# Performance work log

Measured on AMD Instinct MI355X. Metric: run time of the kernel, lower is better.

The kernel has to match this reference:

```python
import jax, jax.numpy as jnp
import numpy as np

B, N, D, H = 8, 1024, 768, 12
HD = D // H  # head_dim = 64


def setup_inputs() -> dict:
    key = jax.random.key(0)
    k1, k2 = jax.random.split(key)
    x = jax.random.normal(k1, (B, N, D), dtype=jnp.float32)
    W_qkv = jax.random.normal(k2, (D, 3 * D), dtype=jnp.float32) * 0.02
    b_qkv = jnp.zeros((3 * D,), dtype=jnp.float32)
    return {"x": x, "W_qkv": W_qkv, "b_qkv": b_qkv}


def reference(x, W_qkv, b_qkv):
    b, n, d = x.shape
    qkv = x @ W_qkv + b_qkv                      # [B, N, 3D]
    qkv = qkv.reshape(b, n, 3, H, HD)
    qkv = jnp.transpose(qkv, (2, 0, 3, 1, 4))    # [3, B, H, N, HD]
    q, k, v = qkv[0], qkv[1], qkv[2]
    scale = 1.0 / jnp.sqrt(jnp.float32(HD))
    scores = jnp.einsum('bhqd,bhkd->bhqk', q, k) * scale   # [B, H, N, N]
    attn = jax.nn.softmax(scores, axis=-1)
    out = jnp.einsum('bhqk,bhkd->bhqd', attn, v)            # [B, H, N, HD]
    # concat heads along last dim (same as torch.cat over head outputs)
    return jnp.transpose(out, (0, 2, 1, 3)).reshape(b, n, d)
```

## Files before the change

kernel.cpp:

```cpp
#include <hip/hip_runtime.h>
#include <stdint.h>

#define BB 8
#define NN 1024
#define DDIM 768
#define HH 12
#define HDIM 64
#define D3 2304
#define MM 8192

typedef __attribute__((ext_vector_type(4))) float f32x4;
typedef __attribute__((ext_vector_type(16))) float f32x16;
typedef __attribute__((ext_vector_type(8))) __bf16 bf16x8;
typedef __attribute__((ext_vector_type(8))) unsigned short u16x8;
typedef __attribute__((ext_vector_type(4))) unsigned short u16x4;

__device__ __forceinline__ unsigned short f2bf(float f) {
  unsigned int u = __float_as_uint(f);
  u += 0x7FFFu + ((u >> 16) & 1u);
  return (unsigned short)(u >> 16);
}

__device__ __forceinline__ void gload_lds16(const void* g, void* l) {
  __builtin_amdgcn_global_load_lds((const __attribute__((address_space(1))) void*)g,
                                   (__attribute__((address_space(3))) void*)l,
                                   16, 0, 0);
}

__device__ __forceinline__ unsigned cvtpk_bf16(float lo, float hi) {
  unsigned r;
  asm("v_cvt_pk_bf16_f32 %0, %1, %2" : "=v"(r) : "v"(lo), "v"(hi));
  return r;
}

__device__ __forceinline__ bf16x8 mkfrag(unsigned a, unsigned b, unsigned c, unsigned d) {
  union { unsigned u[4]; bf16x8 v; } x;
  x.u[0] = a; x.u[1] = b; x.u[2] = c; x.u[3] = d;
  return x.v;
}

#if __has_builtin(__builtin_amdgcn_exp2f)
#define EXP2(x) __builtin_amdgcn_exp2f(x)
#else
#define EXP2(x) exp2f(x)
#endif

#define QSCL 0.18033688f

__global__ void k_prep(const float4* __restrict__ x, u16x4* __restrict__ xb,
                       const float* __restrict__ W, unsigned short* __restrict__ Wt) {
  __shared__ float tile[32][33];
  const int bid = blockIdx.x;
  if (bid < 6144) {
    int i = bid * 256 + threadIdx.x;
    float4 v = x[i];
    u16x4 o;
    o[0] = f2bf(v.x); o[1] = f2bf(v.y); o[2] = f2bf(v.z); o[3] = f2bf(v.w);
    xb[i] = o;
    return;
  }
  const int bid2 = bid - 6144;
  const int tx = threadIdx.x & 31, ty = threadIdx.x >> 5;
  const int n0 = (bid2 % 72) * 32;
  const int k0 = (bid2 / 72) * 32;
  for (int i = 0; i < 4; ++i) {
    int k = k0 + ty + i * 8;
    tile[ty + i * 8][tx] = W[(size_t)k * D3 + n0 + tx];
  }
  __syncthreads();
  for (int i = 0; i < 4; ++i) {
    int n = n0 + ty + i * 8;
    Wt[(size_t)n * DDIM + k0 + tx] = f2bf(tile[tx][ty + i * 8]);
  }
}

__global__ __launch_bounds__(256, 2)
void k_gemm(const unsigned short* __restrict__ A, const unsigned short* __restrict__ Bt,
            const float* __restrict__ bias, unsigned short* __restrict__ qb,
            unsigned short* __restrict__ kp, unsigned short* __restrict__ vp) {
  __shared__ char lds[64 * 1024];
  const int t = threadIdx.x, lane = t & 63, wid = t >> 6;
  const int orig = blockIdx.x;
  const int xcd = orig & 7, tt = orig >> 3;
  const int m0 = (xcd * 8 + (tt & 7)) * 128;
  const int n0 = (tt >> 3) * 128;
  const int wr = wid >> 1, wc = wid & 1;
  const int grp = lane >> 4, lc = lane & 15;

  f32x4 acc[4][4];
  for (int i = 0; i < 4; ++i)
    for (int j = 0; j < 4; ++j) acc[i][j] = (f32x4)(0.0f);

  auto STAGE = [&](int buf, int kt) {
    char* Ab = lds + buf * 32768;
    char* Bb = Ab + 16384;
#pragma unroll
    for (int i = 0; i < 4; ++i) {
      int id = wid * 4 + i;
      int row = id * 8 + (lane >> 3);
      int cs = ((lane & 7) << 4) ^ ((row & 7) << 4);
      gload_lds16((const char*)A + (size_t)(m0 + row) * 1536 + kt * 128 + cs, Ab + id * 1024);
      gload_lds16((const char*)Bt + (size_t)(n0 + row) * 1536 + kt * 128 + cs, Bb + id * 1024);
    }
  };

  STAGE(0, 0);
  for (int kt = 0; kt < 12; ++kt) {
    if (kt < 11) {
      STAGE((kt + 1) & 1, kt + 1);
      asm volatile("s_waitcnt vmcnt(8)" ::: "memory");
    } else {
      asm volatile("s_waitcnt vmcnt(0)" ::: "memory");
    }
    __builtin_amdgcn_s_barrier();

    const char* As = lds + (kt & 1) * 32768;
    const char* Bs = As + 16384;
    bf16x8 af[4][2], bfr[4][2];
#pragma unroll
    for (int f = 0; f < 4; ++f)
#pragma unroll
      for (int kk = 0; kk < 2; ++kk) {
        int ra = wr * 64 + f * 16 + lc;
        af[f][kk] = *(const bf16x8*)(As + ra * 128 + ((kk * 64 + grp * 16) ^ ((ra & 7) << 4)));
        int rb = wc * 64 + f * 16 + lc;
        bfr[f][kk] = *(const bf16x8*)(Bs + rb * 128 + ((kk * 64 + grp * 16) ^ ((rb & 7) << 4)));
      }
    __builtin_amdgcn_s_setprio(1);
#pragma unroll
    for (int mf = 0; mf < 4; ++mf)
#pragma unroll
      for (int nf = 0; nf < 4; ++nf) {
        acc[mf][nf] = __builtin_amdgcn_mfma_f32_16x16x32_bf16(af[mf][0], bfr[nf][0], acc[mf][nf], 0, 0, 0);
        acc[mf][nf] = __builtin_amdgcn_mfma_f32_16x16x32_bf16(af[mf][1], bfr[nf][1], acc[mf][nf], 0, 0, 0);
      }
    __builtin_amdgcn_s_setprio(0);
    __builtin_amdgcn_s_barrier();
  }

  float bv[4];
#pragma unroll
  for (int nf = 0; nf < 4; ++nf) bv[nf] = bias[n0 + wc * 64 + nf * 16 + lc];

  const int nt = n0 >> 7;
  if (nt < 6) {
#pragma unroll
    for (int mf = 0; mf < 4; ++mf)
#pragma unroll
      for (int nf = 0; nf < 4; ++nf)
#pragma unroll
        for (int i = 0; i < 4; ++i) {
          int r = m0 + wr * 64 + mf * 16 + grp * 4 + i;
          int c = n0 + wc * 64 + nf * 16 + lc;
          qb[(size_t)r * DDIM + c] = f2bf((acc[mf][nf][i] + bv[nf]) * QSCL);
        }
  } else {
    __syncthreads();
    unsigned short* lt = (unsigned short*)lds + wid * 4608;
    const int l31 = lane & 31, hi2 = lane >> 5;
    const int bb = m0 >> 10;
    const int kt_ = ((m0 & 1023) >> 6) + wr;
    size_t base;
    unsigned short* dst;
    if (nt < 12) {
      const int h = ((n0 - DDIM) >> 6) + wc;
      base = ((size_t)(bb * HH + h) * 16 + kt_) * 4096;
      dst = kp;
#pragma unroll
      for (int mf = 0; mf < 4; ++mf)
#pragma unroll
        for (int nf = 0; nf < 4; ++nf)
#pragma unroll
          for (int i = 0; i < 4; ++i)
            lt[(mf * 16 + grp * 4 + i) * 72 + nf * 16 + lc] = f2bf(acc[mf][nf][i] + bv[nf]);
    } else {
      const int h = ((n0 - 2 * DDIM) >> 6) + wc;
      base = ((size_t)(bb * HH + h) * 16 + kt_) * 4096;
      dst = vp;
#pragma unroll
      for (int mf = 0; mf < 4; ++mf)
#pragma unroll
        for (int nf = 0; nf < 4; ++nf)
#pragma unroll
          for (int i = 0; i < 4; ++i)
            lt[(nf * 16 + lc) * 72 + mf * 16 + grp * 4 + i] = f2bf(acc[mf][nf][i] + bv[nf]);
    }
    __syncthreads();
#pragma unroll
    for (int c2 = 0; c2 < 4; ++c2)
#pragma unroll
      for (int r = 0; r < 2; ++r)
        *(u16x8*)(dst + base + ((size_t)(c2 * 2 + r) * 64 + lane) * 8) =
          *(const u16x8*)&lt[(r * 32 + l31) * 72 + c2 * 16 + hi2 * 8];
  }
}

__global__ __launch_bounds__(256, 3)
void k_attn(const unsigned short* __restrict__ qb,
            const unsigned short* __restrict__ kp, const unsigned short* __restrict__ vp,
            float* __restrict__ out) {
  __shared__ char lds[32 * 1024];
  const int lane = threadIdx.x & 63, wid = threadIdx.x >> 6;
  const int orig = blockIdx.x;
  const int wg = (orig & 7) * 96 + (orig >> 3);
  const int bh = wg >> 3, qt = wg & 7;
  const int b = bh / HH, h = bh % HH;
  const int q0 = qt * 128 + wid * 32;
  const int l31 = lane & 31, hi = lane >> 5;

  auto STAGE = [&](int bi, int kt2) {
    char* buf = lds + bi * 16384;
    const char* gk = (const char*)kp + (size_t)(bh * 16 + kt2) * 8192 + lane * 16;
    const char* gv = (const char*)vp + (size_t)(bh * 16 + kt2) * 8192 + lane * 16;
#pragma unroll
    for (int i = 0; i < 4; ++i) {
      int e = wid * 4 + i;
      const char* g = (e < 8) ? (gk + e * 1024) : (gv + (e - 8) * 1024);
      char* l = (e < 8) ? (buf + e * 1024) : (buf + 8192 + (e - 8) * 1024);
      gload_lds16(g, l);
    }
  };

  bf16x8 qf[4];
  const char* qbase = (const char*)qb + ((size_t)(b * NN + q0 + l31) * DDIM + h * HDIM) * 2;
#pragma unroll
  for (int ds_ = 0; ds_ < 4; ++ds_)
    qf[ds_] = *(const bf16x8*)(qbase + ds_ * 32 + hi * 16);

  STAGE(0, 0);

  f32x16 acc0 = (f32x16)(0.0f), acc1 = (f32x16)(0.0f);
  float l = 0.0f;

  for (int kt = 0; kt < 16; ++kt) {
    const int cur = kt & 1;
    if (kt < 15) {
      STAGE(cur ^ 1, kt + 1);
      asm volatile("s_waitcnt vmcnt(4)" ::: "memory");
    } else {
      asm volatile("s_waitcnt vmcnt(0)" ::: "memory");
    }
    __builtin_amdgcn_s_barrier();

    const char* Kc = lds + cur * 16384;
    const char* Vc = Kc + 8192;

    bf16x8 kf[4][2];
#pragma unroll
    for (int ds_ = 0; ds_ < 4; ++ds_)
#pragma unroll
      for (int r = 0; r < 2; ++r)
        kf[ds_][r] = *(const bf16x8*)(Kc + (ds_ * 2 + r) * 1024 + lane * 16);

    f32x16 st0 = (f32x16)(0.0f), st1 = (f32x16)(0.0f);
    __builtin_amdgcn_s_setprio(1);
#pragma unroll
    for (int ds_ = 0; ds_ < 4; ++ds_) {
      st0 = __builtin_amdgcn_mfma_f32_32x32x16_bf16(kf[ds_][0], qf[ds_], st0, 0, 0, 0);
      st1 = __builtin_amdgcn_mfma_f32_32x32x16_bf16(kf[ds_][1], qf[ds_], st1, 0, 0, 0);
    }
    __builtin_amdgcn_s_setprio(0);

    bf16x8 vf[4][2];
#pragma unroll
    for (int cc = 0; cc < 4; ++cc)
#pragma unroll
      for (int r = 0; r < 2; ++r)
        vf[cc][r] = *(const bf16x8*)(Vc + (cc * 2 + r) * 1024 + lane * 16);

    float s0 = 0.f, s1 = 0.f, s2 = 0.f, s3 = 0.f;
#pragma unroll
    for (int i = 0; i < 16; i += 4) {
      float p0 = EXP2(st0[i]);
      float p1 = EXP2(st0[i + 1]);
      float p2 = EXP2(st0[i + 2]);
      float p3 = EXP2(st0[i + 3]);
      st0[i] = p0; st0[i + 1] = p1; st0[i + 2] = p2; st0[i + 3] = p3;
      s0 += p0; s1 += p1; s2 += p2; s3 += p3;
    }
#pragma unroll
    for (int i = 0; i < 16; i += 4) {
      float p0 = EXP2(st1[i]);
      float p1 = EXP2(st1[i + 1]);
      float p2 = EXP2(st1[i + 2]);
      float p3 = EXP2(st1[i + 3]);
      st1[i] = p0; st1[i + 1] = p1; st1[i + 2] = p2; st1[i + 3] = p3;
      s0 += p0; s1 += p1; s2 += p2; s3 += p3;
    }
    l += (s0 + s1) + (s2 + s3);

#pragma unroll
    for (int kblk = 0; kblk < 2; ++kblk) {
      const f32x16& sp = kblk ? st1 : st0;
      unsigned c0 = cvtpk_bf16(sp[0], sp[1]),   c1 = cvtpk_bf16(sp[2], sp[3]);
      unsigned c2 = cvtpk_bf16(sp[4], sp[5]),   c3 = cvtpk_bf16(sp[6], sp[7]);
      unsigned c4 = cvtpk_bf16(sp[8], sp[9]),   c5 = cvtpk_bf16(sp[10], sp[11]);
      unsigned c6 = cvtpk_bf16(sp[12], sp[13]), c7 = cvtpk_bf16(sp[14], sp[15]);
      unsigned z0 = hi ? c0 : c2, z1 = hi ? c1 : c3;
      unsigned z2 = hi ? c4 : c6, z3 = hi ? c5 : c7;
      unsigned w0 = __shfl_xor(z0, 32, 64), w1 = __shfl_xor(z1, 32, 64);
      unsigned w2 = __shfl_xor(z2, 32, 64), w3 = __shfl_xor(z3, 32, 64);
      bf16x8 pf0 = mkfrag(hi ? w0 : c0, hi ? w1 : c1, hi ? c2 : w0, hi ? c3 : w1);
      bf16x8 pf1 = mkfrag(hi ? w2 : c4, hi ? w3 : c5, hi ? c6 : w2, hi ? c7 : w3);

      __builtin_amdgcn_s_setprio(1);
#pragma unroll
      for (int ch = 0; ch < 2; ++ch) {
        const int cc = kblk * 2 + ch;
        const bf16x8 pf = ch ? pf1 : pf0;
        acc0 = __builtin_amdgcn_mfma_f32_32x32x16_bf16(vf[cc][0], pf, acc0, 0, 0, 0);
        acc1 = __builtin_amdgcn_mfma_f32_32x32x16_bf16(vf[cc][1], pf, acc1, 0, 0, 0);
      }
      __builtin_amdgcn_s_setprio(0);
    }

    __builtin_amdgcn_s_barrier();
  }

  float lf = l + __shfl_xor(l, 32, 64);
  float inv = 1.0f / lf;
  float* obase = out + (size_t)(b * NN + q0 + l31) * DDIM + h * HDIM + hi * 4;
#pragma unroll
  for (int rq = 0; rq < 4; ++rq) {
    f32x4 o;
    o[0] = acc0[rq * 4] * inv; o[1] = acc0[rq * 4 + 1] * inv;
    o[2] = acc0[rq * 4 + 2] * inv; o[3] = acc0[rq * 4 + 3] * inv;
    *(f32x4*)(obase + rq * 8) = o;
  }
#pragma unroll
  for (int rq = 0; rq < 4; ++rq) {
    f32x4 o;
    o[0] = acc1[rq * 4] * inv; o[1] = acc1[rq * 4 + 1] * inv;
    o[2] = acc1[rq * 4 + 2] * inv; o[3] = acc1[rq * 4 + 3] * inv;
    *(f32x4*)(obase + 32 + rq * 8) = o;
  }
}

extern "C" void kernel_launch(void* const* d_in, const int* in_sizes, int n_in,
                              void* d_out, int out_size, void* d_ws, size_t ws_size,
                              hipStream_t stream) {
  const float* x = (const float*)d_in[0];
  const float* W = (const float*)d_in[1];
  const float* bqkv = (const float*)d_in[2];
  float* out = (float*)d_out;
  char* ws = (char*)d_ws;

  const size_t XB_OFF = 0;
  const size_t WT_OFF = 12582912;
  const size_t QB_OFF = WT_OFF + 3538944;
  const size_t KP_OFF = QB_OFF + 12582912;
  const size_t VP_OFF = KP_OFF + 12582912;
  unsigned short* xb = (unsigned short*)(ws + XB_OFF);
  unsigned short* wt = (unsigned short*)(ws + WT_OFF);
  unsigned short* qbf = (unsigned short*)(ws + QB_OFF);
  unsigned short* kpk = (unsigned short*)(ws + KP_OFF);
  unsigned short* vpk = (unsigned short*)(ws + VP_OFF);

  k_prep<<<dim3(6144 + 1728), dim3(256), 0, stream>>>((const float4*)x, (u16x4*)xb, W, wt);
  k_gemm<<<dim3(1152), dim3(256), 0, stream>>>(xb, wt, bqkv, qbf, kpk, vpk);
  k_attn<<<dim3(768), dim3(256), 0, stream>>>(qbf, kpk, vpk, out);
}
```

Measured before the change: 82.79 us.

## Load K/V fragments directly from global memory instead of LDS double buffering

Removes the LDS double-buffered staging of K and V tiles, along with its barriers and waitcnt handling. Each wave now reads its K and V MFMA fragments straight from global memory, relying on L2/cache reuse across the four waves of a block. The launch bounds hint is also dropped. This removes LDS traffic and block-wide synchronisation, but each wave now issues redundant global loads, and the latency is no longer hidden by explicit prefetch.

Measured after the change: 105.0 us. 26.9% more time.

```diff
diff --git a/kernel.cpp b/kernel.cpp
--- a/kernel.cpp
+++ b/kernel.cpp
@@ -195,11 +195,9 @@
   }
 }
 
-__global__ __launch_bounds__(256, 3)
-void k_attn(const unsigned short* __restrict__ qb,
-            const unsigned short* __restrict__ kp, const unsigned short* __restrict__ vp,
-            float* __restrict__ out) {
-  __shared__ char lds[32 * 1024];
+__global__ void k_attn(const unsigned short* __restrict__ qb,
+                       const unsigned short* __restrict__ kp, const unsigned short* __restrict__ vp,
+                       float* __restrict__ out) {
   const int lane = threadIdx.x & 63, wid = threadIdx.x >> 6;
   const int orig = blockIdx.x;
   const int wg = (orig & 7) * 96 + (orig >> 3);
@@ -208,49 +206,35 @@
   const int q0 = qt * 128 + wid * 32;
   const int l31 = lane & 31, hi = lane >> 5;
 
-  auto STAGE = [&](int bi, int kt2) {
-    char* buf = lds + bi * 16384;
-    const char* gk = (const char*)kp + (size_t)(bh * 16 + kt2) * 8192 + lane * 16;
-    const char* gv = (const char*)vp + (size_t)(bh * 16 + kt2) * 8192 + lane * 16;
-#pragma unroll
-    for (int i = 0; i < 4; ++i) {
-      int e = wid * 4 + i;
-      const char* g = (e < 8) ? (gk + e * 1024) : (gv + (e - 8) * 1024);
-      char* l = (e < 8) ? (buf + e * 1024) : (buf + 8192 + (e - 8) * 1024);
-      gload_lds16(g, l);
-    }
-  };
-
   bf16x8 qf[4];
   const char* qbase = (const char*)qb + ((size_t)(b * NN + q0 + l31) * DDIM + h * HDIM) * 2;
 #pragma unroll
   for (int ds_ = 0; ds_ < 4; ++ds_)
     qf[ds_] = *(const bf16x8*)(qbase + ds_ * 32 + hi * 16);
 
-  STAGE(0, 0);
+  const char* kbase = (const char*)kp + (size_t)bh * 131072 + lane * 16;
+  const char* vbase = (const char*)vp + (size_t)bh * 131072 + lane * 16;
 
   f32x16 acc0 = (f32x16)(0.0f), acc1 = (f32x16)(0.0f);
   float l = 0.0f;
 
   for (int kt = 0; kt < 16; ++kt) {
-    const int cur = kt & 1;
-    if (kt < 15) {
-      STAGE(cur ^ 1, kt + 1);
-      asm volatile("s_waitcnt vmcnt(4)" ::: "memory");
-    } else {
-      asm volatile("s_waitcnt vmcnt(0)" ::: "memory");
-    }
-    __builtin_amdgcn_s_barrier();
-
-    const char* Kc = lds + cur * 16384;
-    const char* Vc = Kc + 8192;
+    const char* kpt = kbase + kt * 8192;
+    const char* vpt = vbase + kt * 8192;
 
     bf16x8 kf[4][2];
 #pragma unroll
     for (int ds_ = 0; ds_ < 4; ++ds_)
 #pragma unroll
       for (int r = 0; r < 2; ++r)
-        kf[ds_][r] = *(const bf16x8*)(Kc + (ds_ * 2 + r) * 1024 + lane * 16);
+        kf[ds_][r] = *(const bf16x8*)(kpt + (ds_ * 2 + r) * 1024);
+
+    bf16x8 vf[4][2];
+#pragma unroll
+    for (int cc = 0; cc < 4; ++cc)
+#pragma unroll
+      for (int r = 0; r < 2; ++r)
+        vf[cc][r] = *(const bf16x8*)(vpt + (cc * 2 + r) * 1024);
 
     f32x16 st0 = (f32x16)(0.0f), st1 = (f32x16)(0.0f);
     __builtin_amdgcn_s_setprio(1);
@@ -260,13 +244,6 @@
       st1 = __builtin_amdgcn_mfma_f32_32x32x16_bf16(kf[ds_][1], qf[ds_], st1, 0, 0, 0);
     }
     __builtin_amdgcn_s_setprio(0);
-
-    bf16x8 vf[4][2];
-#pragma unroll
-    for (int cc = 0; cc < 4; ++cc)
-#pragma unroll
-      for (int r = 0; r < 2; ++r)
-        vf[cc][r] = *(const bf16x8*)(Vc + (cc * 2 + r) * 1024 + lane * 16);
 
     float s0 = 0.f, s1 = 0.f, s2 = 0.f, s3 = 0.f;
 #pragma unroll
@@ -313,8 +290,6 @@
       }
       __builtin_amdgcn_s_setprio(0);
     }
-
-    __builtin_amdgcn_s_barrier();
   }
 
   float lf = l + __shfl_xor(l, 32, 64);
```

## Software-pipeline QK^T one tile ahead with triple-buffered split K/V staging

Applied to the files above, without the earlier changes.

Splits K and V staging into separate triple-buffered LDS regions (48KB total) and prefetches K three tiles and V two tiles ahead. The QK^T MFMAs for the next tile are issued before the softmax and PV of the current tile, using ping-pong score registers, so the exp work can overlap with matrix-core work. The trailing per-iteration barrier is removed and the loop is fully unrolled. The cost is more LDS (which may lower occupancy below the 3-block launch bound) and more live registers.

Result: slower. 217.1 us (+162.2%).

```diff
diff --git a/kernel.cpp b/kernel.cpp
--- a/kernel.cpp
+++ b/kernel.cpp
@@ -199,7 +199,7 @@
 void k_attn(const unsigned short* __restrict__ qb,
             const unsigned short* __restrict__ kp, const unsigned short* __restrict__ vp,
             float* __restrict__ out) {
-  __shared__ char lds[32 * 1024];
+  __shared__ char lds[48 * 1024];
   const int lane = threadIdx.x & 63, wid = threadIdx.x >> 6;
   const int orig = blockIdx.x;
   const int wg = (orig & 7) * 96 + (orig >> 3);
@@ -208,16 +208,22 @@
   const int q0 = qt * 128 + wid * 32;
   const int l31 = lane & 31, hi = lane >> 5;
 
-  auto STAGE = [&](int bi, int kt2) {
-    char* buf = lds + bi * 16384;
+  auto STAGE_K = [&](int bi, int kt2) {
+    char* buf = lds + bi * 8192;
     const char* gk = (const char*)kp + (size_t)(bh * 16 + kt2) * 8192 + lane * 16;
+#pragma unroll
+    for (int i = 0; i < 2; ++i) {
+      int c = wid * 2 + i;
+      gload_lds16(gk + c * 1024, buf + c * 1024);
+    }
+  };
+  auto STAGE_V = [&](int bi, int kt2) {
+    char* buf = lds + 24576 + bi * 8192;
     const char* gv = (const char*)vp + (size_t)(bh * 16 + kt2) * 8192 + lane * 16;
 #pragma unroll
-    for (int i = 0; i < 4; ++i) {
-      int e = wid * 4 + i;
-      const char* g = (e < 8) ? (gk + e * 1024) : (gv + (e - 8) * 1024);
-      char* l = (e < 8) ? (buf + e * 1024) : (buf + 8192 + (e - 8) * 1024);
-      gload_lds16(g, l);
+    for (int i = 0; i < 2; ++i) {
+      int c = wid * 2 + i;
+      gload_lds16(gv + c * 1024, buf + c * 1024);
     }
   };
 
@@ -227,40 +233,61 @@
   for (int ds_ = 0; ds_ < 4; ++ds_)
     qf[ds_] = *(const bf16x8*)(qbase + ds_ * 32 + hi * 16);
 
-  STAGE(0, 0);
+  STAGE_K(0, 0); STAGE_V(0, 0);
+  STAGE_K(1, 1); STAGE_V(1, 1);
+  STAGE_K(2, 2);
 
   f32x16 acc0 = (f32x16)(0.0f), acc1 = (f32x16)(0.0f);
   float l = 0.0f;
 
+  f32x16 stA0 = (f32x16)(0.0f), stA1 = (f32x16)(0.0f);
+  f32x16 stB0 = (f32x16)(0.0f), stB1 = (f32x16)(0.0f);
+
+  asm volatile("s_waitcnt vmcnt(8)" ::: "memory");
+  __builtin_amdgcn_s_barrier();
+  {
+    const char* Kc = lds;
+    __builtin_amdgcn_s_setprio(1);
+#pragma unroll
+    for (int ds_ = 0; ds_ < 4; ++ds_) {
+      bf16x8 k0 = *(const bf16x8*)(Kc + (ds_ * 2 + 0) * 1024 + lane * 16);
+      bf16x8 k1 = *(const bf16x8*)(Kc + (ds_ * 2 + 1) * 1024 + lane * 16);
+      stA0 = __builtin_amdgcn_mfma_f32_32x32x16_bf16(k0, qf[ds_], stA0, 0, 0, 0);
+      stA1 = __builtin_amdgcn_mfma_f32_32x32x16_bf16(k1, qf[ds_], stA1, 0, 0, 0);
+    }
+    __builtin_amdgcn_s_setprio(0);
+  }
+
+#pragma unroll
   for (int kt = 0; kt < 16; ++kt) {
-    const int cur = kt & 1;
+    if (kt < 14)       asm volatile("s_waitcnt vmcnt(4)" ::: "memory");
+    else if (kt == 14) asm volatile("s_waitcnt vmcnt(2)" ::: "memory");
+    else               asm volatile("s_waitcnt vmcnt(0)" ::: "memory");
+    __builtin_amdgcn_s_barrier();
+    if (kt + 3 < 16) STAGE_K((kt + 3) % 3, kt + 3);
+    if (kt + 2 < 16) STAGE_V((kt + 2) % 3, kt + 2);
+
+    const bool even = (kt & 1) == 0;
+    f32x16& sc0 = even ? stA0 : stB0;
+    f32x16& sc1 = even ? stA1 : stB1;
+    f32x16& sn0 = even ? stB0 : stA0;
+    f32x16& sn1 = even ? stB1 : stA1;
+
     if (kt < 15) {
-      STAGE(cur ^ 1, kt + 1);
-      asm volatile("s_waitcnt vmcnt(4)" ::: "memory");
-    } else {
-      asm volatile("s_waitcnt vmcnt(0)" ::: "memory");
-    }
-    __builtin_amdgcn_s_barrier();
-
-    const char* Kc = lds + cur * 16384;
-    const char* Vc = Kc + 8192;
-
-    bf16x8 kf[4][2];
-#pragma unroll
-    for (int ds_ = 0; ds_ < 4; ++ds_)
-#pragma unroll
-      for (int r = 0; r < 2; ++r)
-        kf[ds_][r] = *(const bf16x8*)(Kc + (ds_ * 2 + r) * 1024 + lane * 16);
-
-    f32x16 st0 = (f32x16)(0.0f), st1 = (f32x16)(0.0f);
-    __builtin_amdgcn_s_setprio(1);
-#pragma unroll
-    for (int ds_ = 0; ds_ < 4; ++ds_) {
-      st0 = __builtin_amdgcn_mfma_f32_32x32x16_bf16(kf[ds_][0], qf[ds_], st0, 0, 0, 0);
-      st1 = __builtin_amdgcn_mfma_f32_32x32x16_bf16(kf[ds_][1], qf[ds_], st1, 0, 0, 0);
-    }
-    __builtin_amdgcn_s_setprio(0);
-
+      const char* Kn = lds + ((kt + 1) % 3) * 8192;
+      sn0 = (f32x16)(0.0f); sn1 = (f32x16)(0.0f);
+      __builtin_amdgcn_s_setprio(1);
+#pragma unroll
+      for (int ds_ = 0; ds_ < 4; ++ds_) {
+        bf16x8 k0 = *(const bf16x8*)(Kn + (ds_ * 2 + 0) * 1024 + lane * 16);
+        bf16x8 k1 = *(const bf16x8*)(Kn + (ds_ * 2 + 1) * 1024 + lane * 16);
+        sn0 = __builtin_amdgcn_mfma_f32_32x32x16_bf16(k0, qf[ds_], sn0, 0, 0, 0);
+        sn1 = __builtin_amdgcn_mfma_f32_32x32x16_bf16(k1, qf[ds_], sn1, 0, 0, 0);
+      }
+      __builtin_amdgcn_s_setprio(0);
+    }
+
+    const char* Vc = lds + 24576 + (kt % 3) * 8192;
     bf16x8 vf[4][2];
 #pragma unroll
     for (int cc = 0; cc < 4; ++cc)
@@ -271,27 +298,27 @@
     float s0 = 0.f, s1 = 0.f, s2 = 0.f, s3 = 0.f;
 #pragma unroll
     for (int i = 0; i < 16; i += 4) {
-      float p0 = EXP2(st0[i]);
-      float p1 = EXP2(st0[i + 1]);
-      float p2 = EXP2(st0[i + 2]);
-      float p3 = EXP2(st0[i + 3]);
-      st0[i] = p0; st0[i + 1] = p1; st0[i + 2] = p2; st0[i + 3] = p3;
+      float p0 = EXP2(sc0[i]);
+      float p1 = EXP2(sc0[i + 1]);
+      float p2 = EXP2(sc0[i + 2]);
+      float p3 = EXP2(sc0[i + 3]);
+      sc0[i] = p0; sc0[i + 1] = p1; sc0[i + 2] = p2; sc0[i + 3] = p3;
       s0 += p0; s1 += p1; s2 += p2; s3 += p3;
     }
 #pragma unroll
     for (int i = 0; i < 16; i += 4) {
-      float p0 = EXP2(st1[i]);
-      float p1 = EXP2(st1[i + 1]);
-      float p2 = EXP2(st1[i + 2]);
-      float p3 = EXP2(st1[i + 3]);
-      st1[i] = p0; st1[i + 1] = p1; st1[i + 2] = p2; st1[i + 3] = p3;
+      float p0 = EXP2(sc1[i]);
+      float p1 = EXP2(sc1[i + 1]);
+      float p2 = EXP2(sc1[i + 2]);
+      float p3 = EXP2(sc1[i + 3]);
+      sc1[i] = p0; sc1[i + 1] = p1; sc1[i + 2] = p2; sc1[i + 3] = p3;
       s0 += p0; s1 += p1; s2 += p2; s3 += p3;
     }
     l += (s0 + s1) + (s2 + s3);
 
 #pragma unroll
     for (int kblk = 0; kblk < 2; ++kblk) {
-      const f32x16& sp = kblk ? st1 : st0;
+      const f32x16& sp = kblk ? sc1 : sc0;
       unsigned c0 = cvtpk_bf16(sp[0], sp[1]),   c1 = cvtpk_bf16(sp[2], sp[3]);
       unsigned c2 = cvtpk_bf16(sp[4], sp[5]),   c3 = cvtpk_bf16(sp[6], sp[7]);
       unsigned c4 = cvtpk_bf16(sp[8], sp[9]),   c5 = cvtpk_bf16(sp[10], sp[11]);
@@ -313,8 +340,6 @@
       }
       __builtin_amdgcn_s_setprio(0);
     }
-
-    __builtin_amdgcn_s_barrier();
   }
 
   float lf = l + __shfl_xor(l, 32, 64);
```
